# Optimization experiments

Hardware: AMD Instinct MI355X
Metric: run time of the kernel (lower is better)

The kernel has to match this reference:

```python
import jax, jax.numpy as jnp
import numpy as np

N_LEAVES = 262144  # 2^18, perfect binary tree
INPUT_SIZE = 64
HIDDEN = 128


def setup_inputs() -> dict:
    key = jax.random.key(0)
    ks = jax.random.split(key, 7)
    s_in = 1.0 / np.sqrt(INPUT_SIZE)
    s_h = 1.0 / np.sqrt(HIDDEN)
    return {
        "leaf_x": jax.random.normal(ks[0], (N_LEAVES, INPUT_SIZE), dtype=jnp.float32),
        "W_in": jax.random.uniform(ks[1], (INPUT_SIZE, HIDDEN), jnp.float32, -s_in, s_in),
        "b_in": jax.random.uniform(ks[2], (HIDDEN,), jnp.float32, -s_in, s_in),
        "W_l": jax.random.uniform(ks[3], (HIDDEN, HIDDEN), jnp.float32, -s_h, s_h),
        "b_l": jax.random.uniform(ks[4], (HIDDEN,), jnp.float32, -s_h, s_h),
        "W_r": jax.random.uniform(ks[5], (HIDDEN, HIDDEN), jnp.float32, -s_h, s_h),
        "b_r": jax.random.uniform(ks[6], (HIDDEN,), jnp.float32, -s_h, s_h),
    }


def reference(leaf_x, W_in, b_in, W_l, b_l, W_r, b_r):
    # Leaf rule: h = tanh(input2h(x))  -- batched over all leaves at once.
    h = jnp.tanh(leaf_x @ W_in + b_in)  # [N_LEAVES, HIDDEN]
    # Internal rule: h = tanh(left_h(l) + right_h(r)); note torch adds BOTH
    # linear biases, i.e. b_l + b_r. Perfect binary tree -> batch each depth
    # level as one GEMM pair. Python loop over log2(N) static levels only.
    n = h.shape[0]
    depth = int(np.log2(n))
    for _ in range(depth):
        h = jnp.tanh(h[0::2] @ W_l + h[1::2] @ W_r + (b_l + b_r))
    return h  # root hidden state, shape [1, HIDDEN]
```

## Files before the change

### kernel.cpp

```cpp
#include <hip/hip_runtime.h>
#include <hip/hip_bf16.h>


typedef unsigned short u16;
typedef unsigned int u32;
typedef __attribute__((ext_vector_type(8))) short bf16x8;
typedef __attribute__((ext_vector_type(4))) float f32x4;

#define TANH_S 2.8853900817779268f
#define HS 128

__device__ __forceinline__ u16 f2bf(float f) {
    __hip_bfloat16 h = __float2bfloat16(f);
    return *(u16*)&h;
}
__device__ __forceinline__ u32 f2bf_pk(float a, float b) {
    __hip_bfloat162 h = __float22bfloat162_rn(make_float2(a, b));
    return *(u32*)&h;
}
__device__ __forceinline__ float tanh_ps(float xs) {
#if __has_builtin(__builtin_amdgcn_exp2f) && __has_builtin(__builtin_amdgcn_rcpf)
    float t = __builtin_amdgcn_exp2f(xs);
    float r = __builtin_amdgcn_rcpf(t + 1.0f);
    return __builtin_fmaf(-2.0f, r, 1.0f);
#else
    float e = __expf(xs * 0.6931471805599453f);
    return 1.0f - 2.0f / (e + 1.0f);
#endif
}
__device__ __forceinline__ int swz(int row, int c) {
    return c ^ (((row >> 1) & 7) << 3);
}

#define MFMA16(a, b, c) __builtin_amdgcn_mfma_f32_16x16x32_bf16((a), (b), (c), 0, 0, 0)

#define WS_BWIN 32768
#define WS_L1_BYTE 81920
#define WS_L2_BYTE (WS_L1_BYTE + 4194304)
#define WS_NEED (WS_L2_BYTE + 32768)

__global__ __launch_bounds__(256) void kprep(
    const float* __restrict__ Win, const float* __restrict__ Wl,
    const float* __restrict__ Wr, u16* __restrict__ ws) {
    const int tid = threadIdx.x;
    const int w = tid >> 6, lane = tid & 63, quad = lane >> 4, lq = lane & 15;
    const int c0 = 32 * w + 2 * lq;
    const int part = blockIdx.x;
    if (part < 4) {
#pragma unroll
        for (int kk = 0; kk < 2; ++kk) {
            const int kc = part * 2 + kk;
            const float* W = (kc < 4) ? Wl : Wr;
            const int kbase = (kc & 3) * 32 + quad * 8;
            bf16x8 f0, f1;
#pragma unroll
            for (int j = 0; j < 8; ++j) {
                float2 v = *(const float2*)(W + (size_t)(kbase + j) * 128 + c0);
                f0[j] = (short)f2bf(v.x * TANH_S);
                f1[j] = (short)f2bf(v.y * TANH_S);
            }
            *(bf16x8*)(ws + (kc * 2 + 0) * 2048 + tid * 8) = f0;
            *(bf16x8*)(ws + (kc * 2 + 1) * 2048 + tid * 8) = f1;
        }
    } else {
#pragma unroll
        for (int kc = 0; kc < 2; ++kc) {
            const int kbase = kc * 32 + quad * 8;
            bf16x8 f0, f1;
#pragma unroll
            for (int j = 0; j < 8; ++j) {
                float2 v = *(const float2*)(Win + (size_t)(kbase + j) * 128 + c0);
                f0[j] = (short)f2bf(v.x * TANH_S);
                f1[j] = (short)f2bf(v.y * TANH_S);
            }
            *(bf16x8*)(ws + WS_BWIN + (kc * 2 + 0) * 2048 + tid * 8) = f0;
            *(bf16x8*)(ws + WS_BWIN + (kc * 2 + 1) * 2048 + tid * 8) = f1;
        }
    }
}

__device__ __forceinline__ void load_bw_ws(const u16* __restrict__ ws, int tid,
                                           bf16x8 (&bw)[8][2]) {
#pragma unroll
    for (int kc = 0; kc < 8; ++kc) {
        bw[kc][0] = *(const bf16x8*)(ws + (kc * 2 + 0) * 2048 + tid * 8);
        bw[kc][1] = *(const bf16x8*)(ws + (kc * 2 + 1) * 2048 + tid * 8);
    }
}

template <int M, int Mlast, bool BFOUT>
__device__ __forceinline__ void level_chain(
    u16* in, u16* nxt, const bf16x8 (&bw)[8][2], float bs0, float bs1,
    u16* outB, float* outF, int quad, int lq, int c0) {
    constexpr int ntiles = (M + 15) >> 4;
#pragma unroll
    for (int rt = 0; rt < ntiles; ++rt) {
        const int r0e = rt * 16;
        bf16x8 a[8];
#pragma unroll
        for (int kc = 0; kc < 8; ++kc) {
            const int row = 2 * (r0e + lq) + (kc >> 2);
            const int kb = (kc & 3) * 32 + quad * 8;
            a[kc] = *(const bf16x8*)(in + row * HS + swz(row, kb));
        }
        f32x4 ac0 = {bs0, bs0, bs0, bs0}, ac1 = {bs1, bs1, bs1, bs1};
#pragma unroll
        for (int kc = 0; kc < 8; ++kc) {
            ac0 = MFMA16(a[kc], bw[kc][0], ac0);
            ac1 = MFMA16(a[kc], bw[kc][1], ac1);
        }
#pragma unroll
        for (int r = 0; r < 4; ++r) {
            const int ro = r0e + quad * 4 + r;
            if (ro < M) {
                float v0 = tanh_ps(ac0[r]);
                float v1 = tanh_ps(ac1[r]);
                if constexpr (M == Mlast) {
                    if constexpr (BFOUT) {
                        *(u32*)(outB + ro * 128 + c0) = f2bf_pk(v0, v1);
                    } else {
                        *(float2*)(outF + ro * 128 + c0) = make_float2(v0, v1);
                    }
                } else {
                    *(u32*)(nxt + ro * HS + swz(ro, c0)) = f2bf_pk(v0, v1);
                }
            }
        }
    }
    __syncthreads();
    if constexpr (M > Mlast)
        level_chain<(M >> 1), Mlast, BFOUT>(nxt, in, bw, bs0, bs1,
                                            outB, outF, quad, lq, c0);
}

__global__ __launch_bounds__(256, 3) void kfront(
    const float* XB, const float* __restrict__ bin,
    const float* __restrict__ bl, const float* __restrict__ br,
    const u16* __restrict__ ws, u16* l1, int l1s) {
    __shared__ __align__(16) u16 H0[128 * HS];
    __shared__ __align__(16) u16 POOL[128 * 64];

    const int tid = threadIdx.x;
    const int w = tid >> 6, lane = tid & 63, quad = lane >> 4, lq = lane & 15;
    const int b = blockIdx.x;
    const int c0 = 32 * w + 2 * lq;
    u16* Xa = POOL;
    u16* H1 = POOL;

    const float* Xg = XB + (size_t)b * 8192;
#pragma unroll
    for (int t = 0; t < 8; ++t) {
        int i4 = tid + 256 * t;
        int r = i4 >> 4, k4 = (i4 & 15) << 2;
        float4 v = *(const float4*)(Xg + r * 64 + k4);
        *(uint2*)(Xa + r * 64 + k4) =
            make_uint2(f2bf_pk(v.x, v.y), f2bf_pk(v.z, v.w));
    }

    bf16x8 bwin[2][2];
#pragma unroll
    for (int kc = 0; kc < 2; ++kc) {
        bwin[kc][0] = *(const bf16x8*)(ws + WS_BWIN + (kc * 2 + 0) * 2048 + tid * 8);
        bwin[kc][1] = *(const bf16x8*)(ws + WS_BWIN + (kc * 2 + 1) * 2048 + tid * 8);
    }
    bf16x8 bw[8][2];
    load_bw_ws(ws, tid, bw);

    const float2 binp = *(const float2*)(bin + c0);
    const float2 blp = *(const float2*)(bl + c0);
    const float2 brp = *(const float2*)(br + c0);
    const float bi0 = binp.x * TANH_S, bi1 = binp.y * TANH_S;
    const float bs0 = (blp.x + brp.x) * TANH_S, bs1 = (blp.y + brp.y) * TANH_S;
    __syncthreads();

#pragma unroll
    for (int rt = 0; rt < 8; ++rt) {
        const int r0e = rt * 16;
        const int rowa = r0e + lq;
        bf16x8 a0 = *(const bf16x8*)(Xa + rowa * 64 + quad * 8);
        bf16x8 a1 = *(const bf16x8*)(Xa + rowa * 64 + 32 + quad * 8);
        f32x4 ac0 = {bi0, bi0, bi0, bi0}, ac1 = {bi1, bi1, bi1, bi1};
        ac0 = MFMA16(a0, bwin[0][0], ac0);
        ac0 = MFMA16(a1, bwin[1][0], ac0);
        ac1 = MFMA16(a0, bwin[0][1], ac1);
        ac1 = MFMA16(a1, bwin[1][1], ac1);
#pragma unroll
        for (int r = 0; r < 4; ++r) {
            const int ro = r0e + quad * 4 + r;
            *(u32*)(H0 + ro * HS + swz(ro, c0)) =
                f2bf_pk(tanh_ps(ac0[r]), tanh_ps(ac1[r]));
        }
    }
    __syncthreads();

    level_chain<64, 8, true>(H0, H1, bw, bs0, bs1,
                             l1 + (size_t)b * l1s, nullptr, quad, lq, c0);
}

__global__ __launch_bounds__(256) void kmid(
    const u16* l1, int l1s, const float* __restrict__ bl,
    const float* __restrict__ br, const u16* __restrict__ ws,
    u16* l2, size_t l2s) {
    __shared__ __align__(16) u16 H0[128 * HS];
    __shared__ __align__(16) u16 H1[64 * HS];

    const int tid = threadIdx.x;
    const int w = tid >> 6, lane = tid & 63, quad = lane >> 4, lq = lane & 15;
    const int t = blockIdx.x;
    const int c0 = 32 * w + 2 * lq;

    bf16x8 bw[8][2];
    load_bw_ws(ws, tid, bw);

    const u16* base = l1 + (size_t)(16 * t) * l1s;
#pragma unroll
    for (int it = 0; it < 8; ++it) {
        int i4 = tid + 256 * it;
        int r = i4 >> 4, c8 = (i4 & 15) << 3;
        uint4 v = *(const uint4*)(base + (size_t)(r >> 3) * l1s + (r & 7) * 128 + c8);
        *(uint4*)(H0 + r * HS + swz(r, c8)) = v;
    }
    const float2 blp = *(const float2*)(bl + c0);
    const float2 brp = *(const float2*)(br + c0);
    const float bs0 = (blp.x + brp.x) * TANH_S, bs1 = (blp.y + brp.y) * TANH_S;
    __syncthreads();

    level_chain<64, 1, true>(H0, H1, bw, bs0, bs1,
                             l2 + (size_t)t * l2s, nullptr, quad, lq, c0);
}

__global__ __launch_bounds__(256) void ktail(
    const u16* l2, size_t l2s, const float* __restrict__ bl,
    const float* __restrict__ br, const u16* __restrict__ ws,
    float* __restrict__ out) {
    __shared__ __align__(16) u16 H0[128 * HS];
    __shared__ __align__(16) u16 H1[64 * HS];

    const int tid = threadIdx.x;
    const int w = tid >> 6, lane = tid & 63, quad = lane >> 4, lq = lane & 15;
    const int c0 = 32 * w + 2 * lq;

    bf16x8 bw[8][2];
    load_bw_ws(ws, tid, bw);

#pragma unroll
    for (int it = 0; it < 8; ++it) {
        int i4 = tid + 256 * it;
        int r = i4 >> 4, c8 = (i4 & 15) << 3;
        uint4 v = *(const uint4*)(l2 + (size_t)r * l2s + c8);
        *(uint4*)(H0 + r * HS + swz(r, c8)) = v;
    }
    const float2 blp = *(const float2*)(bl + c0);
    const float2 brp = *(const float2*)(br + c0);
    const float bs0 = (blp.x + brp.x) * TANH_S, bs1 = (blp.y + brp.y) * TANH_S;
    __syncthreads();

    level_chain<64, 1, false>(H0, H1, bw, bs0, bs1, nullptr, out,
                              quad, lq, c0);
}

extern "C" void kernel_launch(void* const* d_in, const int* in_sizes, int n_in,
                              void* d_out, int out_size, void* d_ws, size_t ws_size,
                              hipStream_t stream) {
    float* XB = (float*)d_in[0];
    const float* Win = (const float*)d_in[1];
    const float* bin = (const float*)d_in[2];
    const float* Wl  = (const float*)d_in[3];
    const float* bl  = (const float*)d_in[4];
    const float* Wr  = (const float*)d_in[5];
    const float* br  = (const float*)d_in[6];
    float* out = (float*)d_out;
    u16* ws = (u16*)d_ws;

    const bool big = (d_ws != nullptr) && (ws_size >= (size_t)WS_NEED);
    u16* l1; int l1s; u16* l2; size_t l2s;
    if (big) {
        l1 = (u16*)((char*)d_ws + WS_L1_BYTE); l1s = 1024;
        l2 = (u16*)((char*)d_ws + WS_L2_BYTE); l2s = 128;
    } else {
        l1 = (u16*)XB;        l1s = 16384;
        l2 = (u16*)XB + 8192; l2s = 16 * 16384;
    }

    kprep<<<5, 256, 0, stream>>>(Win, Wl, Wr, ws);
    kfront<<<2048, 256, 0, stream>>>(XB, bin, bl, br, ws, l1, l1s);
    kmid<<<128, 256, 0, stream>>>(l1, l1s, bl, br, ws, l2, l2s);
    ktail<<<1, 256, 0, stream>>>(l2, l2s, bl, br, ws, out);
}
```

Before: 132.9 us.

## Fuse mid and tail tree levels into front kernel via last-block atomic counters

Adds per-group atomic counters so the last of every 16 front blocks gathers the group's level-1 outputs and reduces them, and the last group block then computes the root. This removes the separate kmid and ktail launches and their launch gaps when workspace is large enough. In exchange it adds threadfences and atomics, and the mid-level work now runs on only the 128 last-arriving blocks, which finish at different times.

New measurement: 405.1 us. 3.05x slower.

```diff
diff --git a/kernel.cpp b/kernel.cpp
--- a/kernel.cpp
+++ b/kernel.cpp
@@ -37,15 +37,17 @@
 #define WS_BWIN 32768
 #define WS_L1_BYTE 81920
 #define WS_L2_BYTE (WS_L1_BYTE + 4194304)
-#define WS_NEED (WS_L2_BYTE + 32768)
+#define WS_CNT_BYTE (WS_L2_BYTE + 32768)
+#define WS_NEED (WS_CNT_BYTE + 512)
 
 __global__ __launch_bounds__(256) void kprep(
     const float* __restrict__ Win, const float* __restrict__ Wl,
-    const float* __restrict__ Wr, u16* __restrict__ ws) {
+    const float* __restrict__ Wr, u16* __restrict__ ws, u32* cnts) {
     const int tid = threadIdx.x;
     const int w = tid >> 6, lane = tid & 63, quad = lane >> 4, lq = lane & 15;
     const int c0 = 32 * w + 2 * lq;
     const int part = blockIdx.x;
+    if (part == 4 && cnts && tid < 129) cnts[tid] = 0;
     if (part < 4) {
 #pragma unroll
         for (int kk = 0; kk < 2; ++kk) {
@@ -133,12 +135,24 @@
                                             outB, outF, quad, lq, c0);
 }
 
+__device__ __forceinline__ void gather128c(u16* H0, const u16* src, int tid) {
+#pragma unroll
+    for (int it = 0; it < 8; ++it) {
+        int i4 = tid + 256 * it;
+        int r = i4 >> 4, c8 = (i4 & 15) << 3;
+        uint4 v = *(const uint4*)(src + r * 128 + c8);
+        *(uint4*)(H0 + r * HS + swz(r, c8)) = v;
+    }
+}
+
 __global__ __launch_bounds__(256, 3) void kfront(
     const float* XB, const float* __restrict__ bin,
     const float* __restrict__ bl, const float* __restrict__ br,
-    const u16* __restrict__ ws, u16* l1, int l1s) {
+    const u16* __restrict__ ws, u16* l1, int l1s,
+    u16* l2, u32* cnts, float* out, int fuse) {
     __shared__ __align__(16) u16 H0[128 * HS];
     __shared__ __align__(16) u16 POOL[128 * 64];
+    __shared__ int amlast;
 
     const int tid = threadIdx.x;
     const int w = tid >> 6, lane = tid & 63, quad = lane >> 4, lq = lane & 15;
@@ -195,6 +209,33 @@
 
     level_chain<64, 8, true>(H0, H1, bw, bs0, bs1,
                              l1 + (size_t)b * l1s, nullptr, quad, lq, c0);
+
+    if (!fuse) return;
+
+    __threadfence();
+    __syncthreads();
+    const int g = b >> 4;
+    if (tid == 0) amlast = (atomicAdd(&cnts[g], 1u) == 15u) ? 1 : 0;
+    __syncthreads();
+    if (!amlast) return;
+    __threadfence();
+
+    gather128c(H0, l1 + (size_t)g * 16384, tid);
+    __syncthreads();
+    level_chain<64, 1, true>(H0, H1, bw, bs0, bs1,
+                             l2 + (size_t)g * 128, nullptr, quad, lq, c0);
+
+    __threadfence();
+    __syncthreads();
+    if (tid == 0) amlast = (atomicAdd(&cnts[128], 1u) == 127u) ? 1 : 0;
+    __syncthreads();
+    if (!amlast) return;
+    __threadfence();
+
+    gather128c(H0, l2, tid);
+    __syncthreads();
+    level_chain<64, 1, false>(H0, H1, bw, bs0, bs1, nullptr, out,
+                              quad, lq, c0);
 }
 
 __global__ __launch_bounds__(256) void kmid(
@@ -273,17 +314,24 @@
     u16* ws = (u16*)d_ws;
 
     const bool big = (d_ws != nullptr) && (ws_size >= (size_t)WS_NEED);
-    u16* l1; int l1s; u16* l2; size_t l2s;
+    u16* l1; int l1s; u16* l2; size_t l2s; u32* cnts; int fuse;
     if (big) {
         l1 = (u16*)((char*)d_ws + WS_L1_BYTE); l1s = 1024;
         l2 = (u16*)((char*)d_ws + WS_L2_BYTE); l2s = 128;
+        cnts = (u32*)((char*)d_ws + WS_CNT_BYTE);
+        fuse = 1;
     } else {
         l1 = (u16*)XB;        l1s = 16384;
         l2 = (u16*)XB + 8192; l2s = 16 * 16384;
-    }
-
-    kprep<<<5, 256, 0, stream>>>(Win, Wl, Wr, ws);
-    kfront<<<2048, 256, 0, stream>>>(XB, bin, bl, br, ws, l1, l1s);
-    kmid<<<128, 256, 0, stream>>>(l1, l1s, bl, br, ws, l2, l2s);
-    ktail<<<1, 256, 0, stream>>>(l2, l2s, bl, br, ws, out);
-}
+        cnts = nullptr;
+        fuse = 0;
+    }
+
+    kprep<<<5, 256, 0, stream>>>(Win, Wl, Wr, ws, cnts);
+    kfront<<<2048, 256, 0, stream>>>(XB, bin, bl, br, ws, l1, l1s,
+                                     l2, cnts, out, fuse);
+    if (!fuse) {
+        kmid<<<128, 256, 0, stream>>>(l1, l1s, bl, br, ws, l2, l2s);
+        ktail<<<1, 256, 0, stream>>>(l2, l2s, bl, br, ws, out);
+    }
+}
```
